# Kernel tuning notes

Measured on AMD Instinct MI355X. Metric: run time of the kernel, lower is better.

Reference implementation:

```python
import jax, jax.numpy as jnp
import numpy as np

B, T, E, D, G = 64, 64, 2048, 4096, 8
H3 = 3 * D  # gru projects deter -> 3*deter (reset, cand, update)
EPS = 1e-4  # Norm default eps


def _rms(x, scale):
    # Norm impl='rms': x * rsqrt(mean(x^2, -1) + eps) * scale
    return x * (jax.lax.rsqrt((x * x).mean(-1, keepdims=True) + EPS) * scale)


def setup_inputs() -> dict:
    key = jax.random.key(0)
    ks = jax.random.split(key, 4)
    x = jax.random.normal(ks[0], (B, T, E), jnp.float32)
    deter0 = jax.random.normal(ks[1], (B, D), jnp.float32)
    # dense in-projection: concat(deter, x) -> D, rms norm + silu
    W_in = jax.random.normal(ks[2], (D + E, D), jnp.float32) * (1.0 / np.sqrt(D + E))
    b_in = jnp.zeros((D,), jnp.float32)
    scale_in = jnp.ones((D,), jnp.float32)
    # BlockLinear D -> 3D with G groups; weight (G, D/G, 3D/G), per-block rms scales
    W_blk = jax.random.normal(ks[3], (G, D // G, H3 // G), jnp.float32) * (1.0 / np.sqrt(D // G))
    b_blk = jnp.zeros((H3,), jnp.float32)
    scale_blk = jnp.ones((G, H3 // G), jnp.float32)
    return dict(x=x, deter0=deter0, W_in=W_in, b_in=b_in, scale_in=scale_in,
                W_blk=W_blk, b_blk=b_blk, scale_blk=scale_blk)


def reference(x, deter0, W_in, b_in, scale_in, W_blk, b_blk, scale_blk):
    def step(deter, x_t):
        h = jnp.concatenate([deter, x_t], -1)                # [B, D+E]
        y = jax.nn.silu(_rms(h @ W_in + b_in, scale_in))     # [B, D]
        # block-diagonal GEMM: '...ki,kio->...ko' as in BlockLinear._layer
        z = jnp.einsum('bgi,gio->bgo', y.reshape(B, G, D // G), W_blk)
        z = z.reshape(B, H3) + b_blk
        # block_norm=True: per-block rms over each of the G contiguous chunks
        z = _rms(z.reshape(B, G, H3 // G), scale_blk).reshape(B, H3)
        reset, cand, update = jnp.split(z, 3, -1)
        reset = jax.nn.sigmoid(reset)
        cand = jnp.tanh(reset * cand)
        update = jax.nn.sigmoid(update - 1.0)
        deter = update * cand + (1.0 - update) * deter
        return deter, deter

    _, deters = jax.lax.scan(step, deter0, jnp.swapaxes(x, 0, 1))  # scan over T
    return jnp.swapaxes(deters, 0, 1)  # [B, T, D]
```

## Files before the change

kernel.cpp:

```cpp
#include <hip/hip_runtime.h>

typedef unsigned short u16;
typedef unsigned int u32;
typedef __bf16 bfx8 __attribute__((ext_vector_type(8)));
typedef float f32x4 __attribute__((ext_vector_type(4)));

constexpr int BB = 64;
constexpr int TT = 64;
constexpr int EE = 2048;
constexpr int DD = 4096;
constexpr int GG = 8;
constexpr int H3 = 3 * DD;
constexpr int CH = H3 / GG;
constexpr float EPSf = 1e-4f;

static __device__ __forceinline__ u16 f2bf(float f) {
  u32 u = __builtin_bit_cast(u32, f);
  u32 r = (u + 0x7fffu + ((u >> 16) & 1u)) >> 16;
  return (u16)r;
}


__global__ void __launch_bounds__(256) k_f2b(const float* __restrict__ in,
                                             u16* __restrict__ out, int n4) {
  int i = blockIdx.x * 256 + threadIdx.x;
  int stride = gridDim.x * 256;
  for (; i < n4; i += stride) {
    float4 v = ((const float4*)in)[i];
    uint2 o;
    o.x = (u32)f2bf(v.x) | ((u32)f2bf(v.y) << 16);
    o.y = (u32)f2bf(v.z) | ((u32)f2bf(v.w) << 16);
    ((uint2*)out)[i] = o;
  }
}

__global__ void __launch_bounds__(256) k_initdet(const float* __restrict__ d0,
                                                 float* __restrict__ dF,
                                                 u16* __restrict__ dB, int n4) {
  int i = blockIdx.x * 256 + threadIdx.x;
  if (i < n4) {
    float4 v = ((const float4*)d0)[i];
    ((float4*)dF)[i] = v;
    uint2 o;
    o.x = (u32)f2bf(v.x) | ((u32)f2bf(v.y) << 16);
    o.y = (u32)f2bf(v.z) | ((u32)f2bf(v.w) << 16);
    ((uint2*)dB)[i] = o;
  }
}

__global__ void __launch_bounds__(256) k_transpose_f2b(const float* __restrict__ in,
                                                       u16* __restrict__ out,
                                                       int R, int C) {
  __shared__ float tile[32][33];
  size_t base = (size_t)blockIdx.z * R * C;
  in += base; out += base;
  int tx = threadIdx.x & 31, ty = threadIdx.x >> 5;
  int r0 = blockIdx.y * 32, c0 = blockIdx.x * 32;
#pragma unroll
  for (int i = 0; i < 4; i++) {
    int rr = ty * 4 + i;
    tile[rr][tx] = in[(size_t)(r0 + rr) * C + (c0 + tx)];
  }
  __syncthreads();
#pragma unroll
  for (int i = 0; i < 4; i++) {
    int cc = ty * 4 + i;
    out[(size_t)(c0 + cc) * R + (r0 + tx)] = f2bf(tile[tx][cc]);
  }
}


template<int BM, int BN, int WR, int WC>
__global__ void __launch_bounds__(256) k_gemm(
    const u16* __restrict__ A, int lda,
    const u16* __restrict__ B, int ldb,
    float* __restrict__ C, int ldc,
    const float* __restrict__ bias,
    int K) {
  constexpr int BK = 64, LS = BK + 8;
  constexpr int WTM = BM / WR, WTN = BN / WC, MF = WTM / 16, NF = WTN / 16;
  __shared__ u16 As[BM * LS];
  __shared__ u16 Bs[BN * LS];
  const int tid = threadIdx.x;
  const int m0 = blockIdx.y * BM, n0 = blockIdx.x * BN;
  const int w = tid >> 6, lane = tid & 63;
  const int wr = w / WC, wc = w % WC;
  const int lr = lane & 15, lk = (lane >> 4) * 8;

  f32x4 acc[MF][NF] = {};

  for (int kt = 0; kt < K; kt += BK) {
#pragma unroll
    for (int c = tid; c < BM * 8; c += 256) {
      int row = c >> 3, cc = c & 7;
      *(uint4*)&As[row * LS + cc * 8] =
          *(const uint4*)(A + (size_t)(m0 + row) * lda + kt + cc * 8);
    }
#pragma unroll
    for (int c = tid; c < BN * 8; c += 256) {
      int row = c >> 3, cc = c & 7;
      *(uint4*)&Bs[row * LS + cc * 8] =
          *(const uint4*)(B + (size_t)(n0 + row) * ldb + kt + cc * 8);
    }
    __syncthreads();
#pragma unroll
    for (int kk = 0; kk < BK; kk += 32) {
      bfx8 av[MF], bv[NF];
#pragma unroll
      for (int mi = 0; mi < MF; mi++)
        av[mi] = *(const bfx8*)&As[(wr * WTM + mi * 16 + lr) * LS + kk + lk];
#pragma unroll
      for (int ni = 0; ni < NF; ni++)
        bv[ni] = *(const bfx8*)&Bs[(wc * WTN + ni * 16 + lr) * LS + kk + lk];
#pragma unroll
      for (int mi = 0; mi < MF; mi++)
#pragma unroll
        for (int ni = 0; ni < NF; ni++)
          acc[mi][ni] = __builtin_amdgcn_mfma_f32_16x16x32_bf16(av[mi], bv[ni], acc[mi][ni], 0, 0, 0);
    }
    __syncthreads();
  }

  const int rq = (lane >> 4) * 4;
#pragma unroll
  for (int mi = 0; mi < MF; mi++) {
#pragma unroll
    for (int ni = 0; ni < NF; ni++) {
      int n = n0 + wc * WTN + ni * 16 + lr;
      float bias_v = bias ? bias[n] : 0.f;
#pragma unroll
      for (int r = 0; r < 4; r++) {
        int m = m0 + wr * WTM + mi * 16 + rq + r;
        C[(size_t)m * ldc + n] = acc[mi][ni][r] + bias_v;
      }
    }
  }
}

__global__ void __launch_bounds__(256) kA(const u16* __restrict__ dB,
                                          const u16* __restrict__ WT,
                                          float* __restrict__ part) {
  constexpr int LS = 72;
  __shared__ u16 As[64 * LS];
  __shared__ u16 Bs[64 * LS];
  const int tid = threadIdx.x;
  const int n0 = blockIdx.x * 64;
  const int k0 = blockIdx.y * 512;
  const int w = tid >> 6, lane = tid & 63;
  const int lr = lane & 15, lk = (lane >> 4) * 8, rq = (lane >> 4) * 4;
  const int srow = tid >> 2, sc = (tid & 3) * 8;
  const u16* Arow = dB + (size_t)srow * DD + k0 + sc;
  const u16* Brow = WT + (size_t)(n0 + srow) * (DD + EE) + k0 + sc;

  f32x4 acc[4] = {};
  for (int kt = 0; kt < 512; kt += 64) {
    *(uint4*)&As[srow * LS + sc]      = *(const uint4*)(Arow + kt);
    *(uint4*)&As[srow * LS + sc + 32] = *(const uint4*)(Arow + kt + 32);
    *(uint4*)&Bs[srow * LS + sc]      = *(const uint4*)(Brow + kt);
    *(uint4*)&Bs[srow * LS + sc + 32] = *(const uint4*)(Brow + kt + 32);
    __syncthreads();
#pragma unroll
    for (int kk = 0; kk < 64; kk += 32) {
      bfx8 av = *(const bfx8*)&As[(w * 16 + lr) * LS + kk + lk];
#pragma unroll
      for (int ni = 0; ni < 4; ni++) {
        bfx8 bv = *(const bfx8*)&Bs[(ni * 16 + lr) * LS + kk + lk];
        acc[ni] = __builtin_amdgcn_mfma_f32_16x16x32_bf16(av, bv, acc[ni], 0, 0, 0);
      }
    }
    __syncthreads();
  }
  float* P = part + (size_t)blockIdx.y * BB * DD;
#pragma unroll
  for (int ni = 0; ni < 4; ni++)
#pragma unroll
    for (int r = 0; r < 4; r++)
      P[(size_t)(w * 16 + rq + r) * DD + n0 + ni * 16 + lr] = acc[ni][r];
}

__global__ void __launch_bounds__(256) kB(const float* __restrict__ part,
                                          const float* __restrict__ Xproj,
                                          const float* __restrict__ scale_in,
                                          u16* __restrict__ ybf, int t) {
  const int b = blockIdx.x, tid = threadIdx.x;
  const int w = tid >> 6, lane = tid & 63;
  __shared__ float sred[4];
  const float* xp = Xproj + ((size_t)b * TT + t) * DD;
  const float* pb = part + (size_t)b * DD;
  float4 v[4];
  float ss = 0.f;
#pragma unroll
  for (int j = 0; j < 4; j++) {
    const int col = j * 1024 + tid * 4;
    float4 a = *(const float4*)(xp + col);
#pragma unroll
    for (int kc = 0; kc < 8; kc++) {
      float4 p = *(const float4*)(pb + (size_t)kc * BB * DD + col);
      a.x += p.x; a.y += p.y; a.z += p.z; a.w += p.w;
    }
    v[j] = a;
    ss += a.x * a.x + a.y * a.y + a.z * a.z + a.w * a.w;
  }
#pragma unroll
  for (int o = 32; o > 0; o >>= 1) ss += __shfl_down(ss, o);
  if (lane == 0) sred[w] = ss;
  __syncthreads();
  const float r = rsqrtf((sred[0] + sred[1] + sred[2] + sred[3]) / (float)DD + EPSf);
#pragma unroll
  for (int j = 0; j < 4; j++) {
    const int col = j * 1024 + tid * 4;
    float4 sc4 = *(const float4*)(scale_in + col);
    float y0 = v[j].x * r * sc4.x, y1 = v[j].y * r * sc4.y;
    float y2 = v[j].z * r * sc4.z, y3 = v[j].w * r * sc4.w;
    y0 = y0 / (1.f + __expf(-y0)); y1 = y1 / (1.f + __expf(-y1));
    y2 = y2 / (1.f + __expf(-y2)); y3 = y3 / (1.f + __expf(-y3));
    uint2 o;
    o.x = (u32)f2bf(y0) | ((u32)f2bf(y1) << 16);
    o.y = (u32)f2bf(y2) | ((u32)f2bf(y3) << 16);
    *(uint2*)(ybf + (size_t)b * DD + col) = o;
  }
}

__global__ void __launch_bounds__(256) kC(const u16* __restrict__ ybf,
                                          const u16* __restrict__ WbT,
                                          const float* __restrict__ b_blk,
                                          float* __restrict__ zbuf,
                                          float* __restrict__ zsq) {
  constexpr int LS = 72;
  __shared__ u16 As[64 * LS];
  __shared__ u16 Bs[64 * LS];
  const int tid = threadIdx.x;
  const int wg = blockIdx.x;
  const int n0g = wg * 64;
  const int g = n0g / CH, nl = n0g % CH;
  const int w = tid >> 6, lane = tid & 63;
  const int lr = lane & 15, lk = (lane >> 4) * 8, rq = (lane >> 4) * 4;
  const int srow = tid >> 2, sc = (tid & 3) * 8;
  const u16* Arow = ybf + (size_t)srow * DD + g * (DD / GG) + sc;
  const u16* Brow = WbT + ((size_t)g * CH + nl + srow) * (DD / GG) + sc;

  f32x4 acc[4] = {};
  for (int kt = 0; kt < DD / GG; kt += 64) {
    *(uint4*)&As[srow * LS + sc]      = *(const uint4*)(Arow + kt);
    *(uint4*)&As[srow * LS + sc + 32] = *(const uint4*)(Arow + kt + 32);
    *(uint4*)&Bs[srow * LS + sc]      = *(const uint4*)(Brow + kt);
    *(uint4*)&Bs[srow * LS + sc + 32] = *(const uint4*)(Brow + kt + 32);
    __syncthreads();
#pragma unroll
    for (int kk = 0; kk < 64; kk += 32) {
      bfx8 av = *(const bfx8*)&As[(w * 16 + lr) * LS + kk + lk];
#pragma unroll
      for (int ni = 0; ni < 4; ni++) {
        bfx8 bv = *(const bfx8*)&Bs[(ni * 16 + lr) * LS + kk + lk];
        acc[ni] = __builtin_amdgcn_mfma_f32_16x16x32_bf16(av, bv, acc[ni], 0, 0, 0);
      }
    }
    __syncthreads();
  }
  float sq[4] = {0.f, 0.f, 0.f, 0.f};
#pragma unroll
  for (int ni = 0; ni < 4; ni++) {
    const int n = n0g + ni * 16 + lr;
    const float bias_v = b_blk[n];
#pragma unroll
    for (int r = 0; r < 4; r++) {
      const float zv = acc[ni][r] + bias_v;
      zbuf[(size_t)(w * 16 + rq + r) * H3 + n] = zv;
      sq[r] += zv * zv;
    }
  }
#pragma unroll
  for (int o = 1; o < 16; o <<= 1) {
#pragma unroll
    for (int r = 0; r < 4; r++) sq[r] += __shfl_xor(sq[r], o);
  }
  if (lr == 0) {
#pragma unroll
    for (int r = 0; r < 4; r++) zsq[(size_t)wg * 64 + w * 16 + rq + r] = sq[r];
  }
}

__global__ void __launch_bounds__(256) kD(const float* __restrict__ zbuf,
                                          const float* __restrict__ zsq,
                                          const float* __restrict__ sblk,
                                          float* __restrict__ dF,
                                          u16* __restrict__ dB,
                                          float* __restrict__ out, int t) {
  const int wg = blockIdx.x, tid = threadIdx.x;
  const int b = wg >> 2, s = wg & 3;
  __shared__ float sred[8];
  if (tid < 8) {
    float ssq = 0.f;
    const int j0 = tid * 24;
#pragma unroll
    for (int j = 0; j < 24; j++) ssq += zsq[(size_t)(j0 + j) * 64 + b];
    sred[tid] = rsqrtf(ssq / (float)CH + EPSf);
  }
  __syncthreads();
  const int d0 = s * 1024 + tid * 4;
  const float* zr = zbuf + (size_t)b * H3;
  float4 z0 = *(const float4*)(zr + d0);
  float4 z1 = *(const float4*)(zr + DD + d0);
  float4 z2 = *(const float4*)(zr + 2 * DD + d0);
  float4 dold = *(const float4*)(dF + (size_t)b * DD + d0);
  const float rsA = sred[d0 / CH];
  const float rsB = sred[(DD + d0) / CH];
  const float rsC = sred[(2 * DD + d0) / CH];
  float dn[4];
  const float* z0p = (const float*)&z0;
  const float* z1p = (const float*)&z1;
  const float* z2p = (const float*)&z2;
  const float* dop = (const float*)&dold;
#pragma unroll
  for (int e = 0; e < 4; e++) {
    const int dd = d0 + e;
    const float a0 = z0p[e] * rsA * sblk[dd];
    const float a1 = z1p[e] * rsB * sblk[DD + dd];
    const float a2 = z2p[e] * rsC * sblk[2 * DD + dd];
    const float reset = 1.f / (1.f + __expf(-a0));
    const float cand = tanhf(reset * a1);
    const float upd = 1.f / (1.f + __expf(-(a2 - 1.f)));
    dn[e] = upd * cand + (1.f - upd) * dop[e];
  }
  *(float4*)(dF + (size_t)b * DD + d0) = make_float4(dn[0], dn[1], dn[2], dn[3]);
  uint2 o;
  o.x = (u32)f2bf(dn[0]) | ((u32)f2bf(dn[1]) << 16);
  o.y = (u32)f2bf(dn[2]) | ((u32)f2bf(dn[3]) << 16);
  *(uint2*)(dB + (size_t)b * DD + d0) = o;
  *(float4*)(out + ((size_t)b * TT + t) * DD + d0) = make_float4(dn[0], dn[1], dn[2], dn[3]);
}


extern "C" void kernel_launch(void* const* d_in, const int* in_sizes, int n_in,
                              void* d_out, int out_size, void* d_ws, size_t ws_size,
                              hipStream_t stream) {
  (void)in_sizes; (void)n_in; (void)out_size; (void)ws_size;
  const float* x         = (const float*)d_in[0];
  const float* deter0    = (const float*)d_in[1];
  const float* W_in      = (const float*)d_in[2];
  const float* b_in      = (const float*)d_in[3];
  const float* scale_in  = (const float*)d_in[4];
  const float* W_blk     = (const float*)d_in[5];
  const float* b_blk     = (const float*)d_in[6];
  const float* scale_blk = (const float*)d_in[7];
  float* out = (float*)d_out;

  char* ws = (char*)d_ws;
  size_t off = 0;
  auto alloc = [&](size_t bytes) -> void* {
    void* p = ws + off;
    off += (bytes + 255) & ~(size_t)255;
    return p;
  };
  u16*   WT    = (u16*)alloc((size_t)DD * (DD + EE) * 2);
  u16*   WbT   = (u16*)alloc((size_t)GG * CH * (DD / GG) * 2);
  float* Xproj = (float*)alloc((size_t)BB * TT * DD * 4);
  float* dF    = (float*)alloc((size_t)BB * DD * 4);
  u16*   dB    = (u16*)alloc((size_t)BB * DD * 2);
  char* scratch = (char*)alloc((size_t)BB * TT * EE * 2);
  u16*   xbf  = (u16*)scratch;
  float* part = (float*)scratch;
  size_t o2 = (size_t)8 * BB * DD * 4;
  u16*   ybf  = (u16*)(scratch + o2);
  o2 += (size_t)BB * DD * 2;
  float* zbuf = (float*)(scratch + o2);
  o2 += (size_t)BB * H3 * 4;
  float* zsq  = (float*)(scratch + o2);

  k_f2b<<<dim3(2048), dim3(256), 0, stream>>>(x, xbf, BB * TT * EE / 4);
  k_transpose_f2b<<<dim3(DD / 32, (DD + EE) / 32, 1), dim3(256), 0, stream>>>(W_in, WT, DD + EE, DD);
  k_transpose_f2b<<<dim3(CH / 32, (DD / GG) / 32, GG), dim3(256), 0, stream>>>(W_blk, WbT, DD / GG, CH);
  k_initdet<<<dim3(BB * DD / 4 / 256), dim3(256), 0, stream>>>(deter0, dF, dB, BB * DD / 4);

  k_gemm<128, 128, 2, 2><<<dim3(DD / 128, BB * TT / 128, 1), dim3(256), 0, stream>>>(
      xbf, EE,
      WT + DD, DD + EE,
      Xproj, DD,
      b_in,
      EE);

  for (int t = 0; t < TT; t++) {
    kA<<<dim3(64, 8), dim3(256), 0, stream>>>(dB, WT, part);
    kB<<<dim3(BB), dim3(256), 0, stream>>>(part, Xproj, scale_in, ybf, t);
    kC<<<dim3(192), dim3(256), 0, stream>>>(ybf, WbT, b_blk, zbuf, zsq);
    kD<<<dim3(256), dim3(256), 0, stream>>>(zbuf, zsq, scale_blk, dF, dB, out, t);
  }
}
```

Measured before the change: 1.965 ms.

## Drop split-K in recurrent GEMM, fuse RMS norm and SiLU into block GEMM

The recurrent deter@W GEMM drops its 8-way split-K. It now runs 64 blocks of 512 threads over the full K=4096, with register-prefetched double-buffered LDS tiles. It adds the Xproj slice in its epilogue and writes per-row partial sums of squares. kB is removed: the RMS-norm reduction, scaling, SiLU and bf16 conversion move into the A-tile load of the block GEMM kernel. This saves a launch per step and the partial-sum round trip, but the first GEMM now uses only 64 workgroups on a large GPU, which risks poor occupancy on the serial K loop, and kC recomputes the activations redundantly across its 24 blocks per group.

```diff
diff --git a/kernel.cpp b/kernel.cpp
--- a/kernel.cpp
+++ b/kernel.cpp
@@ -137,91 +137,92 @@
   }
 }
 
-__global__ void __launch_bounds__(256) kA(const u16* __restrict__ dB,
+constexpr int LSA = 136;
+constexpr int ABUF = 64 * LSA;
+
+__global__ void __launch_bounds__(512) kA(const u16* __restrict__ dB,
                                           const u16* __restrict__ WT,
-                                          float* __restrict__ part) {
-  constexpr int LS = 72;
-  __shared__ u16 As[64 * LS];
-  __shared__ u16 Bs[64 * LS];
+                                          const float* __restrict__ Xproj,
+                                          float* __restrict__ preact,
+                                          float* __restrict__ rowsq,
+                                          int t) {
+  __shared__ u16 As[2 * ABUF];
+  __shared__ u16 Bs[2 * ABUF];
   const int tid = threadIdx.x;
   const int n0 = blockIdx.x * 64;
-  const int k0 = blockIdx.y * 512;
   const int w = tid >> 6, lane = tid & 63;
+  const int wr = w >> 1, wc = w & 1;
   const int lr = lane & 15, lk = (lane >> 4) * 8, rq = (lane >> 4) * 4;
-  const int srow = tid >> 2, sc = (tid & 3) * 8;
-  const u16* Arow = dB + (size_t)srow * DD + k0 + sc;
-  const u16* Brow = WT + (size_t)(n0 + srow) * (DD + EE) + k0 + sc;
-
-  f32x4 acc[4] = {};
-  for (int kt = 0; kt < 512; kt += 64) {
-    *(uint4*)&As[srow * LS + sc]      = *(const uint4*)(Arow + kt);
-    *(uint4*)&As[srow * LS + sc + 32] = *(const uint4*)(Arow + kt + 32);
-    *(uint4*)&Bs[srow * LS + sc]      = *(const uint4*)(Brow + kt);
-    *(uint4*)&Bs[srow * LS + sc + 32] = *(const uint4*)(Brow + kt + 32);
-    __syncthreads();
-#pragma unroll
-    for (int kk = 0; kk < 64; kk += 32) {
-      bfx8 av = *(const bfx8*)&As[(w * 16 + lr) * LS + kk + lk];
-#pragma unroll
-      for (int ni = 0; ni < 4; ni++) {
-        bfx8 bv = *(const bfx8*)&Bs[(ni * 16 + lr) * LS + kk + lk];
+  const int r0s = tid >> 4, s0 = (tid & 15) * 8;
+  const int r1s = (tid + 512) >> 4, s1 = s0;
+  const u16* Ag0 = dB + (size_t)r0s * DD + s0;
+  const u16* Ag1 = dB + (size_t)r1s * DD + s1;
+  const u16* Bg0 = WT + (size_t)(n0 + r0s) * (DD + EE) + s0;
+  const u16* Bg1 = WT + (size_t)(n0 + r1s) * (DD + EE) + s1;
+  const int d0 = r0s * LSA + s0, d1 = r1s * LSA + s1;
+
+  f32x4 acc[2] = {};
+
+  uint4 ra0 = *(const uint4*)(Ag0);
+  uint4 ra1 = *(const uint4*)(Ag1);
+  uint4 rb0 = *(const uint4*)(Bg0);
+  uint4 rb1 = *(const uint4*)(Bg1);
+
+  for (int kt = 0; kt < 32; ++kt) {
+    const int p = kt & 1;
+    u16* ab = As + p * ABUF;
+    u16* bb = Bs + p * ABUF;
+    *(uint4*)&ab[d0] = ra0;
+    *(uint4*)&ab[d1] = ra1;
+    *(uint4*)&bb[d0] = rb0;
+    *(uint4*)&bb[d1] = rb1;
+    __syncthreads();
+    if (kt < 31) {
+      const int ko = (kt + 1) * 128;
+      ra0 = *(const uint4*)(Ag0 + ko);
+      ra1 = *(const uint4*)(Ag1 + ko);
+      rb0 = *(const uint4*)(Bg0 + ko);
+      rb1 = *(const uint4*)(Bg1 + ko);
+    }
+#pragma unroll
+    for (int kk = 0; kk < 128; kk += 32) {
+      bfx8 av = *(const bfx8*)&ab[(wr * 16 + lr) * LSA + kk + lk];
+#pragma unroll
+      for (int ni = 0; ni < 2; ni++) {
+        bfx8 bv = *(const bfx8*)&bb[(wc * 32 + ni * 16 + lr) * LSA + kk + lk];
         acc[ni] = __builtin_amdgcn_mfma_f32_16x16x32_bf16(av, bv, acc[ni], 0, 0, 0);
       }
     }
     __syncthreads();
   }
-  float* P = part + (size_t)blockIdx.y * BB * DD;
-#pragma unroll
-  for (int ni = 0; ni < 4; ni++)
+
+  float sq[4] = {0.f, 0.f, 0.f, 0.f};
+#pragma unroll
+  for (int ni = 0; ni < 2; ni++) {
+#pragma unroll
+    for (int r = 0; r < 4; r++) {
+      const int row = wr * 16 + rq + r;
+      const int col = n0 + wc * 32 + ni * 16 + lr;
+      const float v = acc[ni][r] + Xproj[((size_t)row * TT + t) * DD + col];
+      preact[(size_t)row * DD + col] = v;
+      sq[r] += v * v;
+    }
+  }
+#pragma unroll
+  for (int o = 1; o < 16; o <<= 1) {
+#pragma unroll
+    for (int r = 0; r < 4; r++) sq[r] += __shfl_xor(sq[r], o);
+  }
+  if (lr == 0) {
 #pragma unroll
     for (int r = 0; r < 4; r++)
-      P[(size_t)(w * 16 + rq + r) * DD + n0 + ni * 16 + lr] = acc[ni][r];
-}
-
-__global__ void __launch_bounds__(256) kB(const float* __restrict__ part,
-                                          const float* __restrict__ Xproj,
+      rowsq[(size_t)blockIdx.x * 128 + wc * 64 + wr * 16 + rq + r] = sq[r];
+  }
+}
+
+__global__ void __launch_bounds__(256) kC(const float* __restrict__ preact,
+                                          const float* __restrict__ rowsq,
                                           const float* __restrict__ scale_in,
-                                          u16* __restrict__ ybf, int t) {
-  const int b = blockIdx.x, tid = threadIdx.x;
-  const int w = tid >> 6, lane = tid & 63;
-  __shared__ float sred[4];
-  const float* xp = Xproj + ((size_t)b * TT + t) * DD;
-  const float* pb = part + (size_t)b * DD;
-  float4 v[4];
-  float ss = 0.f;
-#pragma unroll
-  for (int j = 0; j < 4; j++) {
-    const int col = j * 1024 + tid * 4;
-    float4 a = *(const float4*)(xp + col);
-#pragma unroll
-    for (int kc = 0; kc < 8; kc++) {
-      float4 p = *(const float4*)(pb + (size_t)kc * BB * DD + col);
-      a.x += p.x; a.y += p.y; a.z += p.z; a.w += p.w;
-    }
-    v[j] = a;
-    ss += a.x * a.x + a.y * a.y + a.z * a.z + a.w * a.w;
-  }
-#pragma unroll
-  for (int o = 32; o > 0; o >>= 1) ss += __shfl_down(ss, o);
-  if (lane == 0) sred[w] = ss;
-  __syncthreads();
-  const float r = rsqrtf((sred[0] + sred[1] + sred[2] + sred[3]) / (float)DD + EPSf);
-#pragma unroll
-  for (int j = 0; j < 4; j++) {
-    const int col = j * 1024 + tid * 4;
-    float4 sc4 = *(const float4*)(scale_in + col);
-    float y0 = v[j].x * r * sc4.x, y1 = v[j].y * r * sc4.y;
-    float y2 = v[j].z * r * sc4.z, y3 = v[j].w * r * sc4.w;
-    y0 = y0 / (1.f + __expf(-y0)); y1 = y1 / (1.f + __expf(-y1));
-    y2 = y2 / (1.f + __expf(-y2)); y3 = y3 / (1.f + __expf(-y3));
-    uint2 o;
-    o.x = (u32)f2bf(y0) | ((u32)f2bf(y1) << 16);
-    o.y = (u32)f2bf(y2) | ((u32)f2bf(y3) << 16);
-    *(uint2*)(ybf + (size_t)b * DD + col) = o;
-  }
-}
-
-__global__ void __launch_bounds__(256) kC(const u16* __restrict__ ybf,
                                           const u16* __restrict__ WbT,
                                           const float* __restrict__ b_blk,
                                           float* __restrict__ zbuf,
@@ -229,22 +230,67 @@
   constexpr int LS = 72;
   __shared__ u16 As[64 * LS];
   __shared__ u16 Bs[64 * LS];
+  __shared__ float red[64][5];
+  __shared__ float rsL[64];
   const int tid = threadIdx.x;
   const int wg = blockIdx.x;
   const int n0g = wg * 64;
-  const int g = n0g / CH, nl = n0g % CH;
+  const int g = wg / 24, nl = n0g - g * CH;
   const int w = tid >> 6, lane = tid & 63;
   const int lr = lane & 15, lk = (lane >> 4) * 8, rq = (lane >> 4) * 4;
-  const int srow = tid >> 2, sc = (tid & 3) * 8;
-  const u16* Arow = ybf + (size_t)srow * DD + g * (DD / GG) + sc;
-  const u16* Brow = WbT + ((size_t)g * CH + nl + srow) * (DD / GG) + sc;
+
+  {
+    const int r = tid >> 2, p = tid & 3;
+    float s = 0.f;
+#pragma unroll
+    for (int i = 0; i < 16; i++) {
+      const int nt = p * 16 + i;
+      s += rowsq[(size_t)nt * 128 + r] + rowsq[(size_t)nt * 128 + 64 + r];
+    }
+    red[r][p] = s;
+  }
+  __syncthreads();
+  if (tid < 64)
+    rsL[tid] = rsqrtf((red[tid][0] + red[tid][1] + red[tid][2] + red[tid][3]) / (float)DD + EPSf);
+  __syncthreads();
+
+  const int arow = tid >> 2, acb = (tid & 3) * 16;
+  const float* Ap = preact + (size_t)arow * DD + g * 512 + acb;
+  const float* Sp = scale_in + g * 512 + acb;
+  const u16* Brow = WbT + ((size_t)g * CH + nl + (tid >> 2)) * 512 + (tid & 3) * 8;
+  const int bdst = (tid >> 2) * LS + (tid & 3) * 8;
 
   f32x4 acc[4] = {};
-  for (int kt = 0; kt < DD / GG; kt += 64) {
-    *(uint4*)&As[srow * LS + sc]      = *(const uint4*)(Arow + kt);
-    *(uint4*)&As[srow * LS + sc + 32] = *(const uint4*)(Arow + kt + 32);
-    *(uint4*)&Bs[srow * LS + sc]      = *(const uint4*)(Brow + kt);
-    *(uint4*)&Bs[srow * LS + sc + 32] = *(const uint4*)(Brow + kt + 32);
+  for (int kt = 0; kt < 512; kt += 64) {
+    const float rr = rsL[arow];
+    float4 f0 = *(const float4*)(Ap + kt);
+    float4 f1 = *(const float4*)(Ap + kt + 4);
+    float4 f2 = *(const float4*)(Ap + kt + 8);
+    float4 f3 = *(const float4*)(Ap + kt + 12);
+    float4 s0 = *(const float4*)(Sp + kt);
+    float4 s1 = *(const float4*)(Sp + kt + 4);
+    float4 s2 = *(const float4*)(Sp + kt + 8);
+    float4 s3 = *(const float4*)(Sp + kt + 12);
+    float yv[16];
+    yv[0] = f0.x * rr * s0.x; yv[1] = f0.y * rr * s0.y; yv[2] = f0.z * rr * s0.z; yv[3] = f0.w * rr * s0.w;
+    yv[4] = f1.x * rr * s1.x; yv[5] = f1.y * rr * s1.y; yv[6] = f1.z * rr * s1.z; yv[7] = f1.w * rr * s1.w;
+    yv[8] = f2.x * rr * s2.x; yv[9] = f2.y * rr * s2.y; yv[10] = f2.z * rr * s2.z; yv[11] = f2.w * rr * s2.w;
+    yv[12] = f3.x * rr * s3.x; yv[13] = f3.y * rr * s3.y; yv[14] = f3.z * rr * s3.z; yv[15] = f3.w * rr * s3.w;
+    uint4 o0, o1;
+    u32* po0 = (u32*)&o0; u32* po1 = (u32*)&o1;
+#pragma unroll
+    for (int j = 0; j < 4; j++) {
+      float a = yv[2 * j], b = yv[2 * j + 1];
+      a = a / (1.f + __expf(-a)); b = b / (1.f + __expf(-b));
+      po0[j] = (u32)f2bf(a) | ((u32)f2bf(b) << 16);
+      float c = yv[8 + 2 * j], d = yv[8 + 2 * j + 1];
+      c = c / (1.f + __expf(-c)); d = d / (1.f + __expf(-d));
+      po1[j] = (u32)f2bf(c) | ((u32)f2bf(d) << 16);
+    }
+    *(uint4*)&As[arow * LS + acb] = o0;
+    *(uint4*)&As[arow * LS + acb + 8] = o1;
+    *(uint4*)&Bs[bdst] = *(const uint4*)(Brow + kt);
+    *(uint4*)&Bs[bdst + 32] = *(const uint4*)(Brow + kt + 32);
     __syncthreads();
 #pragma unroll
     for (int kk = 0; kk < 64; kk += 32) {
@@ -257,6 +303,7 @@
     }
     __syncthreads();
   }
+
   float sq[4] = {0.f, 0.f, 0.f, 0.f};
 #pragma unroll
   for (int ni = 0; ni < 4; ni++) {
@@ -359,10 +406,10 @@
   u16*   dB    = (u16*)alloc((size_t)BB * DD * 2);
   char* scratch = (char*)alloc((size_t)BB * TT * EE * 2);
   u16*   xbf  = (u16*)scratch;
-  float* part = (float*)scratch;
-  size_t o2 = (size_t)8 * BB * DD * 4;
-  u16*   ybf  = (u16*)(scratch + o2);
-  o2 += (size_t)BB * DD * 2;
+  float* preact = (float*)scratch;
+  size_t o2 = (size_t)BB * DD * 4;
+  float* rowsq = (float*)(scratch + o2);
+  o2 += (size_t)64 * 128 * 4;
   float* zbuf = (float*)(scratch + o2);
   o2 += (size_t)BB * H3 * 4;
   float* zsq  = (float*)(scratch + o2);
@@ -380,9 +427,8 @@
       EE);
 
   for (int t = 0; t < TT; t++) {
-    kA<<<dim3(64, 8), dim3(256), 0, stream>>>(dB, WT, part);
-    kB<<<dim3(BB), dim3(256), 0, stream>>>(part, Xproj, scale_in, ybf, t);
-    kC<<<dim3(192), dim3(256), 0, stream>>>(ybf, WbT, b_blk, zbuf, zsq);
+    kA<<<dim3(64), dim3(512), 0, stream>>>(dB, WT, Xproj, preact, rowsq, t);
+    kC<<<dim3(192), dim3(256), 0, stream>>>(preact, rowsq, scale_in, WbT, b_blk, zbuf, zsq);
     kD<<<dim3(256), dim3(256), 0, stream>>>(zbuf, zsq, scale_blk, dF, dB, out, t);
   }
 }
```

New measurement: 3.294 ms. 1.68x slower.
